# Optimization experiments

Hardware: AMD Instinct MI355X
Metric: run time of the kernel (lower is better)

## Reference

```python
import jax, jax.numpy as jnp
import numpy as np

K = 32
BN_EPS = 1e-5


def _fps(points, n_samples):
    # Sequential farthest point sampling; deterministic start at index 0
    # (torch version uses a random start; math otherwise identical).
    B, N, _ = points.shape

    def step(carry, _):
        dist_min, far = carry                                   # (B,N), (B,)
        c = jnp.take_along_axis(points, far[:, None, None].astype(jnp.int32) * jnp.ones((1, 1, 3), jnp.int32), axis=1)  # (B,1,3)
        d = jnp.sum((points - c) ** 2, axis=2)                  # (B,N)
        dist_min = jnp.minimum(dist_min, d)
        return (dist_min, jnp.argmax(dist_min, axis=1)), far

    init = (jnp.full((B, N), 1e10, points.dtype), jnp.zeros((B,), jnp.int64).astype(jnp.int32))
    _, cent = jax.lax.scan(step, init, None, length=n_samples)  # (n_samples, B)
    return cent.T                                               # (B, n_samples)


def _knn_idx(cntrds, pnts, k):
    # squared euclidean distance (same neighbor ordering as torch.cdist)
    d2 = (jnp.sum(cntrds ** 2, -1)[:, :, None]
          + jnp.sum(pnts ** 2, -1)[:, None, :]
          - 2.0 * jnp.einsum('bsc,bnc->bsn', cntrds, pnts))     # (B,ns,N)
    _, idx = jax.lax.top_k(-d2, k)                              # smallest-k
    return idx                                                  # (B,ns,k)


def _gather(x, idx):
    # x: (B,N,D), idx: (B,...) -> (B,...,D)
    return jax.vmap(lambda a, i: a[i])(x, idx)


def _conv1x1(x, w):
    # x: (B,Cin,ns,k), w: (Cout,Cin)
    return jnp.einsum('oc,bcnk->bonk', w, x)


def _bn_relu(x, g, b):
    # training-mode BatchNorm2d (biased variance over B,ns,k) + ReLU
    mean = jnp.mean(x, axis=(0, 2, 3), keepdims=True)
    var = jnp.var(x, axis=(0, 2, 3), keepdims=True)
    xh = (x - mean) * jax.lax.rsqrt(var + BN_EPS)
    return jax.nn.relu(xh * g[None, :, None, None] + b[None, :, None, None])


def setup_inputs() -> dict:
    key = jax.random.key(0)
    ks = jax.random.split(key, 16)
    B, N = 4, 4096
    s = 0.05
    return {
        'p': jax.random.normal(ks[0], (B, N, 3), jnp.float32),
        'f': jax.random.normal(ks[1], (B, 3, N), jnp.float32),
        'w1': jax.random.normal(ks[2], (256, 6), jnp.float32) * s,
        'w2': jax.random.normal(ks[3], (256, 256), jnp.float32) * s,
        'b2': jax.random.normal(ks[4], (256,), jnp.float32) * s,
        'g2': jnp.ones((256,), jnp.float32),
        'be2': jnp.zeros((256,), jnp.float32),
        'w3': jax.random.normal(ks[5], (512, 512), jnp.float32) * s,
        'g3': jnp.ones((512,), jnp.float32),
        'be3': jnp.zeros((512,), jnp.float32),
        'w4': jax.random.normal(ks[6], (256, 512), jnp.float32) * s,
        'g4': jnp.ones((256,), jnp.float32),
        'be4': jnp.zeros((256,), jnp.float32),
    }


def reference(p, f, w1, w2, b2, g2, be2, w3, g3, be3, w4, g4, be4):
    B, N, _ = p.shape
    ns = N // 4
    idx_c = _fps(p, ns)                                   # (B,ns)
    cntrd = _gather(p, idx_c)                             # (B,ns,3)
    feats = jnp.transpose(f, (0, 2, 1))                   # (B,N,3)
    knn = _knn_idx(cntrd, p, K)                           # (B,ns,K)
    dp = _gather(p, knn)                                  # (B,ns,K,3)
    fj = _gather(feats, knn)                              # (B,ns,K,3)
    x = jnp.transpose(jnp.concatenate([dp, fj], -1), (0, 3, 1, 2))  # (B,6,ns,K)
    # conv1: 6->256 (no bias), 256->256 (bias) + BN + ReLU
    x = _conv1x1(x, w1)
    x = _conv1x1(x, w2) + b2[None, :, None, None]
    x = _bn_relu(x, g2, be2)                              # (B,256,ns,K)
    xm = jnp.max(x, axis=-1, keepdims=True)
    x = jnp.concatenate([jnp.broadcast_to(xm, x.shape), x], axis=1)  # (B,512,ns,K)
    # conv2: 512->512 BN ReLU, 512->256 BN ReLU
    x = _bn_relu(_conv1x1(x, w3), g3, be3)
    x = _bn_relu(_conv1x1(x, w4), g4, be4)
    out_feat = jnp.max(x, axis=-1)                        # (B,256,ns)
    return cntrd, out_feat
```

## Files before the change

### kernel.cpp

```cpp
#include <hip/hip_runtime.h>
#include <hip/hip_bf16.h>

#define B_ 4
#define N_ 4096
#define NS_ 1024
#define KNN_ 32
#define NPOS_ 131072
#define BN_EPS_ 1e-5f

using bf16 = __hip_bfloat16;
typedef unsigned short us;
typedef __attribute__((ext_vector_type(8))) short short8;
typedef __attribute__((ext_vector_type(4))) float f32x4;
typedef unsigned long long ull;

__device__ __forceinline__ float bf2f(bf16 h){ return __bfloat162float(h); }
__device__ __forceinline__ us f2bfbits(float x){
    bf16 h = __float2bfloat16(x);
    return *reinterpret_cast<us*>(&h);
}
__device__ __forceinline__ float bits2f(us u){
    unsigned v = ((unsigned)u)<<16; return __uint_as_float(v);
}
__device__ __forceinline__ void unpack8(uint4 v, float* f){
    f[0]=__uint_as_float((v.x&0xFFFFu)<<16); f[1]=__uint_as_float(v.x&0xFFFF0000u);
    f[2]=__uint_as_float((v.y&0xFFFFu)<<16); f[3]=__uint_as_float(v.y&0xFFFF0000u);
    f[4]=__uint_as_float((v.z&0xFFFFu)<<16); f[5]=__uint_as_float(v.z&0xFFFF0000u);
    f[6]=__uint_as_float((v.w&0xFFFFu)<<16); f[7]=__uint_as_float(v.w&0xFFFF0000u);
}
__device__ __forceinline__ uint4 pack8(const float* f){
    uint4 v;
    v.x = (unsigned)f2bfbits(f[0]) | ((unsigned)f2bfbits(f[1])<<16);
    v.y = (unsigned)f2bfbits(f[2]) | ((unsigned)f2bfbits(f[3])<<16);
    v.z = (unsigned)f2bfbits(f[4]) | ((unsigned)f2bfbits(f[5])<<16);
    v.w = (unsigned)f2bfbits(f[6]) | ((unsigned)f2bfbits(f[7])<<16);
    return v;
}
__device__ __forceinline__ unsigned fmono(float v){
    unsigned u = __float_as_uint(v);
    return (u & 0x80000000u) ? ~u : (u | 0x80000000u);
}

template<int CTRL, int ROWM>
__device__ __forceinline__ float dppmaxf(float x){
    int xi = __float_as_int(x);
    int yi = __builtin_amdgcn_update_dpp(xi, xi, CTRL, ROWM, 0xF, false);
    return fmaxf(x, __int_as_float(yi));
}
template<int CTRL, int ROWM>
__device__ __forceinline__ float dppminf(float x){
    int xi = __float_as_int(x);
    int yi = __builtin_amdgcn_update_dpp(xi, xi, CTRL, ROWM, 0xF, false);
    return fminf(x, __int_as_float(yi));
}
__device__ __forceinline__ float wave_max_f32(float x){
    x = dppmaxf<0x111,0xF>(x);
    x = dppmaxf<0x112,0xF>(x);
    x = dppmaxf<0x114,0xF>(x);
    x = dppmaxf<0x118,0xF>(x);
    x = dppmaxf<0x142,0xA>(x);
    x = dppmaxf<0x143,0xC>(x);
    return __int_as_float(__builtin_amdgcn_readlane(__float_as_int(x), 63));
}
__device__ __forceinline__ float wave_min_f32(float x){
    x = dppminf<0x111,0xF>(x);
    x = dppminf<0x112,0xF>(x);
    x = dppminf<0x114,0xF>(x);
    x = dppminf<0x118,0xF>(x);
    x = dppminf<0x142,0xA>(x);
    x = dppminf<0x143,0xC>(x);
    return __int_as_float(__builtin_amdgcn_readlane(__float_as_int(x), 63));
}
__device__ __forceinline__ float rowsum16(float x){
    x += __int_as_float(__builtin_amdgcn_update_dpp(0, __float_as_int(x), 0x111, 0xF, 0xF, true));
    x += __int_as_float(__builtin_amdgcn_update_dpp(0, __float_as_int(x), 0x112, 0xF, 0xF, true));
    x += __int_as_float(__builtin_amdgcn_update_dpp(0, __float_as_int(x), 0x114, 0xF, 0xF, true));
    x += __int_as_float(__builtin_amdgcn_update_dpp(0, __float_as_int(x), 0x118, 0xF, 0xF, true));
    return x;
}
__device__ __forceinline__ float wave_sum_f32(float x){
    x = rowsum16(x);
    x += __int_as_float(__builtin_amdgcn_update_dpp(0, __float_as_int(x), 0x142, 0xA, 0xF, false));
    x += __int_as_float(__builtin_amdgcn_update_dpp(0, __float_as_int(x), 0x143, 0xC, 0xF, false));
    return __int_as_float(__builtin_amdgcn_readlane(__float_as_int(x), 63));
}
__device__ __forceinline__ float max16(const float* v){
    float a = fmaxf(fmaxf(fmaxf(v[0],v[1]),v[2]),v[3]);
    float b = fmaxf(fmaxf(fmaxf(v[4],v[5]),v[6]),v[7]);
    float c = fmaxf(fmaxf(fmaxf(v[8],v[9]),v[10]),v[11]);
    float d = fmaxf(fmaxf(fmaxf(v[12],v[13]),v[14]),v[15]);
    return fmaxf(fmaxf(a,b), fmaxf(c,d));
}
__device__ __forceinline__ float min16(const float* v){
    float a = fminf(fminf(fminf(v[0],v[1]),v[2]),v[3]);
    float b = fminf(fminf(fminf(v[4],v[5]),v[6]),v[7]);
    float c = fminf(fminf(fminf(v[8],v[9]),v[10]),v[11]);
    float d = fminf(fminf(fminf(v[12],v[13]),v[14]),v[15]);
    return fminf(fminf(a,b), fminf(c,d));
}

#define NSLOT 64

__global__ __launch_bounds__(256) void bn_coef(const float* __restrict__ part,
                                               const float* __restrict__ g,
                                               const float* __restrict__ be,
                                               int chbase, int C,
                                               float2* __restrict__ ab){
    int c = blockIdx.x*256 + threadIdx.x;
    if (c < C){
        const float* ps = part + (size_t)(chbase+c)*2*NSLOT;
        float s = 0.f, q = 0.f;
        #pragma unroll 8
        for (int i=0;i<NSLOT;i++){ s += ps[i]; q += ps[NSLOT+i]; }
        const float inv = 1.0f/(float)NPOS_;
        float mean = s*inv;
        float var  = q*inv - mean*mean;
        float a = g[c]*rsqrtf(var + BN_EPS_);
        ab[c] = make_float2(a, be[c] - mean*a);
    }
}

__global__ __launch_bounds__(256) void mega_kernel(const float* __restrict__ p,
                                                   const float* __restrict__ f,
                                                   float* __restrict__ cntrd,
                                                   float* __restrict__ part,
                                                   int* __restrict__ prog,
                                                   int* __restrict__ w26flag,
                                                   const float* __restrict__ w1,
                                                   const float* __restrict__ w2,
                                                   float* __restrict__ W26,
                                                   const float* __restrict__ b2,
                                                   const float* __restrict__ w3,
                                                   us* __restrict__ whi3,
                                                   const float* __restrict__ w4,
                                                   us* __restrict__ whi4,
                                                   bf16* __restrict__ z2){
    __shared__ float4 pxyz[N_];
    __shared__ ull warr[2][4];
    __shared__ int knnS[32];
    __shared__ float Ws[6][256];
    __shared__ float xs[6][32];
    __shared__ int ciS;
    const int bid = blockIdx.x;
    const int t = threadIdx.x;
    const int lane = t & 63;
    const int wave = t >> 6;

    if (bid < 4){
        const int b = bid;
        const float* pb = p + (size_t)b*N_*3;
        float rx[16], ry[16], rz[16], dist[16];
        #pragma unroll
        for (int j=0;j<16;j++){
            int i = t*16+j;
            float x = pb[i*3+0];
            float y = pb[i*3+1];
            float z = pb[i*3+2];
            rx[j]=x; ry[j]=y; rz[j]=z;
            pxyz[i] = make_float4(x,y,z,0.f);
            dist[j]=1e10f;
        }
        __syncthreads();
        float4 c = pxyz[0];
        if (t==0){
            atomicExch(&prog[b*NS_], 1);
            cntrd[(size_t)(b*NS_)*3+0] = c.x;
            cntrd[(size_t)(b*NS_)*3+1] = c.y;
            cntrd[(size_t)(b*NS_)*3+2] = c.z;
        }
        for (int s=1; s<NS_; s++){
            #pragma unroll
            for (int j=0;j<16;j++){
                float dx = __fsub_rn(rx[j],c.x);
                float dy = __fsub_rn(ry[j],c.y);
                float dz = __fsub_rn(rz[j],c.z);
                float d  = __fadd_rn(__fadd_rn(__fmul_rn(dx,dx),__fmul_rn(dy,dy)),__fmul_rn(dz,dz));
                dist[j] = fminf(dist[j], d);
            }
            float lmax = max16(dist);
            float wmax = wave_max_f32(lmax);
            unsigned msk = 0;
            #pragma unroll
            for (int j=0;j<16;j++) msk |= (dist[j]==wmax) ? (1u<<j) : 0u;
            ull ball = __ballot(msk != 0);
            int srclane = (int)__builtin_ctzll(ball);
            unsigned lmsk = (unsigned)__builtin_amdgcn_readlane((int)msk, srclane);
            int widx = (wave*64 + srclane)*16 + (int)__builtin_ctz(lmsk);
            if (lane==0)
                warr[s&1][wave] = ((ull)__float_as_uint(wmax)<<32) | (0xFFFFFFFFu - (unsigned)widx);
            __syncthreads();
            ull g0 = warr[s&1][0], g1 = warr[s&1][1], g2 = warr[s&1][2], g3 = warr[s&1][3];
            ull ga = g0 > g1 ? g0 : g1;
            ull gb = g2 > g3 ? g2 : g3;
            ull g  = ga > gb ? ga : gb;
            int cur = (int)(0xFFFFFFFFu - (unsigned)(g & 0xFFFFFFFFull));
            c = pxyz[cur];
            if (t==0){
                atomicExch(&prog[b*NS_+s], cur+1);
                cntrd[(size_t)(b*NS_+s)*3+0] = c.x;
                cntrd[(size_t)(b*NS_+s)*3+1] = c.y;
                cntrd[(size_t)(b*NS_+s)*3+2] = c.z;
            }
        }
        return;
    }
    if (bid == 4){
        float acc[6] = {0,0,0,0,0,0};
        for (int k=0;k<256;k++){
            float w2v = w2[t*256+k];
            #pragma unroll
            for (int j=0;j<6;j++) acc[j] = fmaf(w2v, w1[k*6+j], acc[j]);
        }
        #pragma unroll
        for (int j=0;j<6;j++) W26[j*256+t] = acc[j];
        __syncthreads();
        if (t==0){ __threadfence(); atomicExch(w26flag, 1); }
        return;
    }
    if (bid < 1029){
        int i = (bid-5)*256 + t;
        whi3[i] = f2bfbits(w3[i]);
        return;
    }
    if (bid < 1541){
        int i = (bid-1029)*256 + t;
        whi4[i] = f2bfbits(w4[i]);
        return;
    }
    const int wid = bid - 1541;
    const int b = wid & 3;
    const int si = wid >> 2;
    const int sidx = b*NS_ + si;
    const float* pb = p + (size_t)b*N_*3;
    if (t == 0){
        int v;
        while ((v = atomicAdd(&prog[sidx], 0)) == 0) {}
        ciS = v - 1;
    }
    __syncthreads();
    const int ci = ciS;
    float cx = pb[ci*3+0];
    float cy = pb[ci*3+1];
    float cz = pb[ci*3+2];
    float c2 = __fadd_rn(__fadd_rn(__fmul_rn(cx,cx),__fmul_rn(cy,cy)),__fmul_rn(cz,cz));
    float d2[16];
    #pragma unroll
    for (int j=0;j<16;j++){
        int i = t*16+j;
        float x = pb[i*3+0];
        float y = pb[i*3+1];
        float z = pb[i*3+2];
        float p2 = __fadd_rn(__fadd_rn(__fmul_rn(x,x),__fmul_rn(y,y)),__fmul_rn(z,z));
        float dot= __fadd_rn(__fadd_rn(__fmul_rn(cx,x),__fmul_rn(cy,y)),__fmul_rn(cz,z));
        d2[j] = __fsub_rn(__fadd_rn(c2,p2), __fmul_rn(2.0f,dot));
    }
    for (int it=0; it<KNN_; it++){
        float lmin = min16(d2);
        float wmin = wave_min_f32(lmin);
        unsigned msk = 0;
        #pragma unroll
        for (int j=0;j<16;j++) msk |= (d2[j]==wmin) ? (1u<<j) : 0u;
        ull ball = __ballot(msk != 0);
        int srclane = (int)__builtin_ctzll(ball);
        unsigned lmsk = (unsigned)__builtin_amdgcn_readlane((int)msk, srclane);
        int widx = (wave*64 + srclane)*16 + (int)__builtin_ctz(lmsk);
        if (lane==0)
            warr[it&1][wave] = ((ull)fmono(wmin)<<32) | (unsigned)widx;
        __syncthreads();
        ull g0 = warr[it&1][0], g1 = warr[it&1][1], g2 = warr[it&1][2], g3 = warr[it&1][3];
        ull ga = g0 < g1 ? g0 : g1;
        ull gb = g2 < g3 ? g2 : g3;
        ull g  = ga < gb ? ga : gb;
        int idx = (int)(g & 0xFFFFFFFFull);
        if ((idx>>4)==t) d2[idx & 15] = INFINITY;
        if (t==0) knnS[it] = idx;
    }
    if (t == 0){ while (atomicAdd(w26flag, 0) == 0) {} __threadfence(); }
    __syncthreads();
    #pragma unroll
    for (int r=0;r<6;r++) Ws[r][t] = W26[r*256+t];
    if (t < 32){
        int i = knnS[t];
        const float* fb = f + (size_t)b*3*N_;
        xs[0][t] = pb[i*3+0];
        xs[1][t] = pb[i*3+1];
        xs[2][t] = pb[i*3+2];
        xs[3][t] = fb[0*N_+i];
        xs[4][t] = fb[1*N_+i];
        xs[5][t] = fb[2*N_+i];
    }
    __syncthreads();
    float w0=Ws[0][t], w1v=Ws[1][t], w2v=Ws[2][t], w3v=Ws[3][t], w4v=Ws[4][t], w5v=Ws[5][t];
    float bias = b2[t];
    bf16* zrow = z2 + (size_t)t*NPOS_ + (size_t)sidx*KNN_;
    float ssum = 0.f, sq = 0.f;
    for (int k0=0;k0<32;k0+=8){
        float y[8];
        #pragma unroll
        for (int u=0;u<8;u++){
            int k = k0+u;
            float acc = bias;
            acc = fmaf(w0, xs[0][k], acc);
            acc = fmaf(w1v,xs[1][k], acc);
            acc = fmaf(w2v,xs[2][k], acc);
            acc = fmaf(w3v,xs[3][k], acc);
            acc = fmaf(w4v,xs[4][k], acc);
            acc = fmaf(w5v,xs[5][k], acc);
            float vr = bits2f(f2bfbits(acc));
            ssum += vr; sq = fmaf(vr, vr, sq);
            y[u] = acc;
        }
        *reinterpret_cast<uint4*>(zrow + k0) = pack8(y);
    }
    const int slot = wid & (NSLOT-1);
    atomicAdd(&part[(size_t)(t*2+0)*NSLOT + slot], ssum);
    atomicAdd(&part[(size_t)(t*2+1)*NSLOT + slot], sq);
}

__global__ __launch_bounds__(256) void xm_kernel(const bf16* __restrict__ z2raw,
                                                 const float2* __restrict__ ab,
                                                 bf16* __restrict__ xm){
    int gid = blockIdx.x*256 + threadIdx.x;
    int c = gid >> 12;
    int bs = gid & 4095;
    float2 s = ab[c];
    const uint4* xp = reinterpret_cast<const uint4*>(z2raw + (size_t)c*NPOS_ + (size_t)bs*KNN_);
    float m = 0.0f;
    #pragma unroll
    for (int r=0;r<4;r++){
        uint4 v = xp[r];
        float fv[8]; unpack8(v, fv);
        #pragma unroll
        for (int u=0;u<8;u++) m = fmaxf(m, fmaf(fv[u], s.x, s.y));
    }
    xm[(size_t)c*4096 + bs] = __float2bfloat16(m);
}

__global__ __launch_bounds__(256) void gemm128(const float* __restrict__ A, int lda, int aoff,
                                               const bf16* __restrict__ B,
                                               int M, int N, int K,
                                               float* __restrict__ Cf){
    __shared__ float As[16][128];
    __shared__ float Bs[16][128];
    const int tid = threadIdx.x;
    const int tx = tid & 15, ty = tid >> 4;
    const int m0 = blockIdx.y*128, n0 = blockIdx.x*128;
    float acc[8][8];
    #pragma unroll
    for (int i=0;i<8;i++)
        #pragma unroll
        for (int j=0;j<8;j++) acc[i][j]=0.f;
    const int arow = tid >> 1, akg = tid & 1;
    const int bkk = tid >> 4, bng = tid & 15;
    for (int k0=0;k0<K;k0+=16){
        const float* aptr = A + (size_t)(m0+arow)*lda + aoff + k0 + akg*8;
        float4 a0 = *reinterpret_cast<const float4*>(aptr);
        float4 a1 = *reinterpret_cast<const float4*>(aptr+4);
        As[akg*8+0][arow]=a0.x; As[akg*8+1][arow]=a0.y;
        As[akg*8+2][arow]=a0.z; As[akg*8+3][arow]=a0.w;
        As[akg*8+4][arow]=a1.x; As[akg*8+5][arow]=a1.y;
        As[akg*8+6][arow]=a1.z; As[akg*8+7][arow]=a1.w;
        uint4 bv = *reinterpret_cast<const uint4*>(B + (size_t)(k0+bkk)*N + n0 + bng*8);
        float bf[8]; unpack8(bv, bf);
        *reinterpret_cast<float4*>(&Bs[bkk][bng*8+0]) = make_float4(bf[0],bf[1],bf[2],bf[3]);
        *reinterpret_cast<float4*>(&Bs[bkk][bng*8+4]) = make_float4(bf[4],bf[5],bf[6],bf[7]);
        __syncthreads();
        #pragma unroll
        for (int kk=0;kk<16;kk++){
            float a[8], b[8];
            *reinterpret_cast<float4*>(&a[0]) = *reinterpret_cast<float4*>(&As[kk][ty*8+0]);
            *reinterpret_cast<float4*>(&a[4]) = *reinterpret_cast<float4*>(&As[kk][ty*8+4]);
            *reinterpret_cast<float4*>(&b[0]) = *reinterpret_cast<float4*>(&Bs[kk][tx*8+0]);
            *reinterpret_cast<float4*>(&b[4]) = *reinterpret_cast<float4*>(&Bs[kk][tx*8+4]);
            #pragma unroll
            for (int i=0;i<8;i++)
                #pragma unroll
                for (int j=0;j<8;j++)
                    acc[i][j] = fmaf(a[i], b[j], acc[i][j]);
        }
        __syncthreads();
    }
    const int n = n0 + tx*8;
    #pragma unroll
    for (int i=0;i<8;i++){
        int m = m0 + ty*8 + i;
        *reinterpret_cast<float4*>(Cf + (size_t)m*N + n + 0) = make_float4(acc[i][0],acc[i][1],acc[i][2],acc[i][3]);
        *reinterpret_cast<float4*>(Cf + (size_t)m*N + n + 4) = make_float4(acc[i][4],acc[i][5],acc[i][6],acc[i][7]);
    }
}

#define LDK 40
__global__ __launch_bounds__(256) void gemm_mfma(const us* __restrict__ Whi,
                                                 int ldw, int aoff,
                                                 const bf16* __restrict__ act, int K,
                                                 const float2* __restrict__ ab,
                                                 bf16* __restrict__ out,
                                                 const float* __restrict__ t3,
                                                 float* __restrict__ part, int chbase){
    __shared__ __align__(16) us AsH[128*LDK];
    __shared__ __align__(16) us Bs [128*LDK];
    __shared__ float t3s[128][4];
    const us* actu = reinterpret_cast<const us*>(act);
    const int t = threadIdx.x;
    const int m0 = blockIdx.x*128, n0 = blockIdx.y*128;
    const int wave = t>>6, lane = t&63;
    const int wm = wave>>1, wn = wave&1;
    const int q = lane>>4, col = lane&15;

    if (t3 && t < 128){
        const float* src = t3 + (size_t)(m0+t)*4096 + (n0>>5);
        t3s[t][0]=src[0]; t3s[t][1]=src[1]; t3s[t][2]=src[2]; t3s[t][3]=src[3];
    }

    f32x4 acc[4][4];
    #pragma unroll
    for (int i=0;i<4;i++)
        #pragma unroll
        for (int j=0;j<4;j++) acc[i][j] = (f32x4){0.f,0.f,0.f,0.f};

    const int ar = t>>1, ah = t&1;
    const int bn = t&127, bh = t>>7;

    for (int k0=0;k0<K;k0+=32){
        const us* sh = Whi + (size_t)(m0+ar)*ldw + aoff + k0 + ah*16;
        uint4 h0 = *reinterpret_cast<const uint4*>(sh);
        uint4 h1 = *reinterpret_cast<const uint4*>(sh+8);
        *reinterpret_cast<uint4*>(&AsH[ar*LDK + ah*16 + 0]) = h0;
        *reinterpret_cast<uint4*>(&AsH[ar*LDK + ah*16 + 8]) = h1;
        us bvals[16];
        #pragma unroll
        for (int j=0;j<16;j++){
            int k = k0 + bh*16 + j;
            float x = bits2f(actu[(size_t)k*NPOS_ + n0 + bn]);
            float2 s = ab[k];
            bvals[j] = f2bfbits(fmaxf(fmaf(x, s.x, s.y), 0.0f));
        }
        *reinterpret_cast<uint4*>(&Bs[bn*LDK + bh*16 + 0]) = *reinterpret_cast<uint4*>(&bvals[0]);
        *reinterpret_cast<uint4*>(&Bs[bn*LDK + bh*16 + 8]) = *reinterpret_cast<uint4*>(&bvals[8]);
        __syncthreads();
        short8 bf[4], afh[4];
        #pragma unroll
        for (int tn=0;tn<4;tn++)
            bf[tn] = *reinterpret_cast<const short8*>(&Bs[(wn*64+tn*16+col)*LDK + q*8]);
        #pragma unroll
        for (int tm=0;tm<4;tm++)
            afh[tm] = *reinterpret_cast<const short8*>(&AsH[(wm*64+tm*16+col)*LDK + q*8]);
        #pragma unroll
        for (int tm=0;tm<4;tm++)
            #pragma unroll
            for (int tn=0;tn<4;tn++)
                acc[tm][tn] = __builtin_amdgcn_mfma_f32_16x16x32_bf16(afh[tm], bf[tn], acc[tm][tn], 0, 0, 0);
        __syncthreads();
    }
    const int slot = (int)(blockIdx.y & (NSLOT-1));
    #pragma unroll
    for (int tm=0;tm<4;tm++){
        #pragma unroll
        for (int r=0;r<4;r++){
            int m_l = wm*64 + tm*16 + q*4 + r;
            float srow = 0.f, qrow = 0.f;
            #pragma unroll
            for (int tn=0;tn<4;tn++){
                int n_l = wn*64 + tn*16 + col;
                float vv = acc[tm][tn][r];
                if (t3) vv += t3s[m_l][n_l>>5];
                us hb = f2bfbits(vv);
                reinterpret_cast<us*>(out)[(size_t)(m0+m_l)*NPOS_ + n0 + n_l] = hb;
                float vr = bits2f(hb);
                srow += vr; qrow = fmaf(vr, vr, qrow);
            }
            srow = rowsum16(srow);
            qrow = rowsum16(qrow);
            if (col == 15){
                atomicAdd(&part[(size_t)((chbase + m0 + m_l)*2+0)*NSLOT + slot], srow);
                atomicAdd(&part[(size_t)((chbase + m0 + m_l)*2+1)*NSLOT + slot], qrow);
            }
        }
    }
}

__global__ __launch_bounds__(256) void final_kernel(const bf16* __restrict__ z4,
                                                    const float* __restrict__ part,
                                                    const float* __restrict__ g4,
                                                    const float* __restrict__ be4,
                                                    float* __restrict__ out){
    __shared__ float abS[2];
    const int t = threadIdx.x;
    const int c = (blockIdx.x >> 2) & 255;
    const int b = blockIdx.x >> 10;
    const int s = ((blockIdx.x & 3) << 8) | t;
    if (t < 64){
        float ss = part[(size_t)((768+c)*2+0)*NSLOT + t];
        float qq = part[(size_t)((768+c)*2+1)*NSLOT + t];
        ss = wave_sum_f32(ss);
        qq = wave_sum_f32(qq);
        if (t==0){
            const float inv = 1.0f/(float)NPOS_;
            float mean = ss*inv;
            float var  = qq*inv - mean*mean;
            float a = g4[c]*rsqrtf(var + BN_EPS_);
            abS[0] = a; abS[1] = be4[c] - mean*a;
        }
    }
    __syncthreads();
    const float a = abS[0], bb = abS[1];
    const int bsi = b*NS_ + s;
    const uint4* zp = reinterpret_cast<const uint4*>(z4 + (size_t)c*NPOS_ + (size_t)bsi*KNN_);
    float m = 0.0f;
    #pragma unroll
    for (int r=0;r<4;r++){
        uint4 v = zp[r];
        float fv[8]; unpack8(v, fv);
        #pragma unroll
        for (int u=0;u<8;u++) m = fmaxf(m, fmaf(fv[u], a, bb));
    }
    out[(size_t)(b*256 + c)*NS_ + s] = m;
}

extern "C" void kernel_launch(void* const* d_in, const int* in_sizes, int n_in,
                              void* d_out, int out_size, void* d_ws, size_t ws_size,
                              hipStream_t stream) {
    const float* p   = (const float*)d_in[0];
    const float* f   = (const float*)d_in[1];
    const float* w1  = (const float*)d_in[2];
    const float* w2  = (const float*)d_in[3];
    const float* b2  = (const float*)d_in[4];
    const float* g2  = (const float*)d_in[5];
    const float* be2 = (const float*)d_in[6];
    const float* w3  = (const float*)d_in[7];
    const float* g3  = (const float*)d_in[8];
    const float* be3 = (const float*)d_in[9];
    const float* w4  = (const float*)d_in[10];
    const float* g4  = (const float*)d_in[11];
    const float* be4 = (const float*)d_in[12];

    char* ws = (char*)d_ws;
    float*  W26  = (float*)(ws + 540672);
    float2* ab2  = (float2*)(ws + 555008);
    float2* ab3  = (float2*)(ws + 557056);
    us* whi3 = (us*)(ws + 561152);
    us* whi4 = (us*)(ws + 1609728);
    float*  t3   = (float*)(ws + 2134016);
    bf16*   z2   = (bf16*)(ws + 10522624);
    bf16*   xm   = (bf16*)(ws + 77631488);
    bf16*   z3   = (bf16*)(ws + 79728640);
    float*  part = (float*)(ws + 213946368);
    int*    prog = (int*)(ws + 214470656);
    int*    w26flag = (int*)(ws + 214487040);
    bf16*   z4   = z2;

    float* out_cntrd = (float*)d_out;
    float* out_feat  = (float*)d_out + (size_t)B_*NS_*3;

    hipMemsetAsync(ws + 213946368, 0, 540676, stream);
    mega_kernel<<<5637, 256, 0, stream>>>(p, f, out_cntrd, part, prog, w26flag,
                                          w1, w2, W26, b2,
                                          w3, whi3, w4, whi4, z2);
    bn_coef<<<1, 256, 0, stream>>>(part, g2, be2, 0, 256, ab2);
    xm_kernel<<<4096, 256, 0, stream>>>(z2, ab2, xm);
    gemm128<<<dim3(32,4), 256, 0, stream>>>(w3, 512, 0, xm, 512, 4096, 256, t3);
    gemm_mfma<<<dim3(4,1024), 256, 0, stream>>>(whi3, 512, 256, z2, 256, ab2, z3, t3, part, 256);
    bn_coef<<<2, 256, 0, stream>>>(part, g3, be3, 256, 512, ab3);
    gemm_mfma<<<dim3(2,1024), 256, 0, stream>>>(whi4, 512, 0, z3, 512, ab3, z4, nullptr, part, 768);
    final_kernel<<<4096, 256, 0, stream>>>(z4, part, g4, be4, out_feat);
}
```

Baseline: 1.056 ms.

## Track per-neighbourhood raw max/min to skip re-reading full activations for max-pool

Since BN followed by ReLU is a monotone affine map per channel, the max over K neighbours can be taken from the raw max (positive scale) or raw min (negative scale). The producers now emit per-position max and min in bf16, and xm_kernel and final_kernel read those instead of the full 32-wide rows. The last GEMM no longer writes its full z4 output. Separately, the FPS blocks get raised wave priority and the spin-wait loops get s_sleep. The trade is extra reductions and stores inside the producer epilogues in exchange for much less read traffic.

```diff
diff --git a/kernel.cpp b/kernel.cpp
--- a/kernel.cpp
+++ b/kernel.cpp
@@ -76,6 +76,20 @@
     x += __int_as_float(__builtin_amdgcn_update_dpp(0, __float_as_int(x), 0x112, 0xF, 0xF, true));
     x += __int_as_float(__builtin_amdgcn_update_dpp(0, __float_as_int(x), 0x114, 0xF, 0xF, true));
     x += __int_as_float(__builtin_amdgcn_update_dpp(0, __float_as_int(x), 0x118, 0xF, 0xF, true));
+    return x;
+}
+__device__ __forceinline__ float rowmax16(float x){
+    x = dppmaxf<0x111,0xF>(x);
+    x = dppmaxf<0x112,0xF>(x);
+    x = dppmaxf<0x114,0xF>(x);
+    x = dppmaxf<0x118,0xF>(x);
+    return x;
+}
+__device__ __forceinline__ float rowmin16(float x){
+    x = dppminf<0x111,0xF>(x);
+    x = dppminf<0x112,0xF>(x);
+    x = dppminf<0x114,0xF>(x);
+    x = dppminf<0x118,0xF>(x);
     return x;
 }
 __device__ __forceinline__ float wave_sum_f32(float x){
@@ -134,7 +148,9 @@
                                                    us* __restrict__ whi3,
                                                    const float* __restrict__ w4,
                                                    us* __restrict__ whi4,
-                                                   bf16* __restrict__ z2){
+                                                   bf16* __restrict__ z2,
+                                                   us* __restrict__ mx2,
+                                                   us* __restrict__ mn2){
     __shared__ float4 pxyz[N_];
     __shared__ ull warr[2][4];
     __shared__ int knnS[32];
@@ -147,6 +163,7 @@
     const int wave = t >> 6;
 
     if (bid < 4){
+        __builtin_amdgcn_s_setprio(3);
         const int b = bid;
         const float* pb = p + (size_t)b*N_*3;
         float rx[16], ry[16], rz[16], dist[16];
@@ -234,7 +251,7 @@
     const float* pb = p + (size_t)b*N_*3;
     if (t == 0){
         int v;
-        while ((v = atomicAdd(&prog[sidx], 0)) == 0) {}
+        while ((v = atomicAdd(&prog[sidx], 0)) == 0) { __builtin_amdgcn_s_sleep(8); }
         ciS = v - 1;
     }
     __syncthreads();
@@ -275,7 +292,7 @@
         if ((idx>>4)==t) d2[idx & 15] = INFINITY;
         if (t==0) knnS[it] = idx;
     }
-    if (t == 0){ while (atomicAdd(w26flag, 0) == 0) {} __threadfence(); }
+    if (t == 0){ while (atomicAdd(w26flag, 0) == 0) { __builtin_amdgcn_s_sleep(8); } __threadfence(); }
     __syncthreads();
     #pragma unroll
     for (int r=0;r<6;r++) Ws[r][t] = W26[r*256+t];
@@ -294,6 +311,7 @@
     float bias = b2[t];
     bf16* zrow = z2 + (size_t)t*NPOS_ + (size_t)sidx*KNN_;
     float ssum = 0.f, sq = 0.f;
+    float mxv = -3.4e38f, mnv = 3.4e38f;
     for (int k0=0;k0<32;k0+=8){
         float y[8];
         #pragma unroll
@@ -308,32 +326,28 @@
             acc = fmaf(w5v,xs[5][k], acc);
             float vr = bits2f(f2bfbits(acc));
             ssum += vr; sq = fmaf(vr, vr, sq);
+            mxv = fmaxf(mxv, vr); mnv = fminf(mnv, vr);
             y[u] = acc;
         }
         *reinterpret_cast<uint4*>(zrow + k0) = pack8(y);
     }
+    mx2[(size_t)t*4096 + sidx] = f2bfbits(mxv);
+    mn2[(size_t)t*4096 + sidx] = f2bfbits(mnv);
     const int slot = wid & (NSLOT-1);
     atomicAdd(&part[(size_t)(t*2+0)*NSLOT + slot], ssum);
     atomicAdd(&part[(size_t)(t*2+1)*NSLOT + slot], sq);
 }
 
-__global__ __launch_bounds__(256) void xm_kernel(const bf16* __restrict__ z2raw,
+__global__ __launch_bounds__(256) void xm_kernel(const us* __restrict__ mx2,
+                                                 const us* __restrict__ mn2,
                                                  const float2* __restrict__ ab,
                                                  bf16* __restrict__ xm){
     int gid = blockIdx.x*256 + threadIdx.x;
     int c = gid >> 12;
-    int bs = gid & 4095;
     float2 s = ab[c];
-    const uint4* xp = reinterpret_cast<const uint4*>(z2raw + (size_t)c*NPOS_ + (size_t)bs*KNN_);
-    float m = 0.0f;
-    #pragma unroll
-    for (int r=0;r<4;r++){
-        uint4 v = xp[r];
-        float fv[8]; unpack8(v, fv);
-        #pragma unroll
-        for (int u=0;u<8;u++) m = fmaxf(m, fmaf(fv[u], s.x, s.y));
-    }
-    xm[(size_t)c*4096 + bs] = __float2bfloat16(m);
+    float x = (s.x >= 0.f) ? bits2f(mx2[gid]) : bits2f(mn2[gid]);
+    float m = fmaxf(fmaf(x, s.x, s.y), 0.0f);
+    xm[gid] = __float2bfloat16(m);
 }
 
 __global__ __launch_bounds__(256) void gemm128(const float* __restrict__ A, int lda, int aoff,
@@ -396,7 +410,9 @@
                                                  const float2* __restrict__ ab,
                                                  bf16* __restrict__ out,
                                                  const float* __restrict__ t3,
-                                                 float* __restrict__ part, int chbase){
+                                                 float* __restrict__ part, int chbase,
+                                                 us* __restrict__ mxout,
+                                                 us* __restrict__ mnout){
     __shared__ __align__(16) us AsH[128*LDK];
     __shared__ __align__(16) us Bs [128*LDK];
     __shared__ float t3s[128][4];
@@ -459,14 +475,17 @@
         for (int r=0;r<4;r++){
             int m_l = wm*64 + tm*16 + q*4 + r;
             float srow = 0.f, qrow = 0.f;
+            float vr4[4];
             #pragma unroll
             for (int tn=0;tn<4;tn++){
                 int n_l = wn*64 + tn*16 + col;
                 float vv = acc[tm][tn][r];
                 if (t3) vv += t3s[m_l][n_l>>5];
                 us hb = f2bfbits(vv);
-                reinterpret_cast<us*>(out)[(size_t)(m0+m_l)*NPOS_ + n0 + n_l] = hb;
+                if (!mxout)
+                    reinterpret_cast<us*>(out)[(size_t)(m0+m_l)*NPOS_ + n0 + n_l] = hb;
                 float vr = bits2f(hb);
+                vr4[tn] = vr;
                 srow += vr; qrow = fmaf(vr, vr, qrow);
             }
             srow = rowsum16(srow);
@@ -475,11 +494,26 @@
                 atomicAdd(&part[(size_t)((chbase + m0 + m_l)*2+0)*NSLOT + slot], srow);
                 atomicAdd(&part[(size_t)((chbase + m0 + m_l)*2+1)*NSLOT + slot], qrow);
             }
-        }
-    }
-}
-
-__global__ __launch_bounds__(256) void final_kernel(const bf16* __restrict__ z4,
+            if (mxout){
+                #pragma unroll
+                for (int h=0;h<2;h++){
+                    float mxl = fmaxf(vr4[2*h], vr4[2*h+1]);
+                    float mnl = fminf(vr4[2*h], vr4[2*h+1]);
+                    mxl = rowmax16(mxl);
+                    mnl = rowmin16(mnl);
+                    if (col == 15){
+                        int bsi = (n0>>5) + wn*2 + h;
+                        mxout[(size_t)(m0+m_l)*4096 + bsi] = f2bfbits(mxl);
+                        mnout[(size_t)(m0+m_l)*4096 + bsi] = f2bfbits(mnl);
+                    }
+                }
+            }
+        }
+    }
+}
+
+__global__ __launch_bounds__(256) void final_kernel(const us* __restrict__ mx4,
+                                                    const us* __restrict__ mn4,
                                                     const float* __restrict__ part,
                                                     const float* __restrict__ g4,
                                                     const float* __restrict__ be4,
@@ -505,16 +539,8 @@
     __syncthreads();
     const float a = abS[0], bb = abS[1];
     const int bsi = b*NS_ + s;
-    const uint4* zp = reinterpret_cast<const uint4*>(z4 + (size_t)c*NPOS_ + (size_t)bsi*KNN_);
-    float m = 0.0f;
-    #pragma unroll
-    for (int r=0;r<4;r++){
-        uint4 v = zp[r];
-        float fv[8]; unpack8(v, fv);
-        #pragma unroll
-        for (int u=0;u<8;u++) m = fmaxf(m, fmaf(fv[u], a, bb));
-    }
-    out[(size_t)(b*256 + c)*NS_ + s] = m;
+    float x = (a >= 0.f) ? bits2f(mx4[(size_t)c*4096 + bsi]) : bits2f(mn4[(size_t)c*4096 + bsi]);
+    out[(size_t)(b*256 + c)*NS_ + s] = fmaxf(fmaf(x, a, bb), 0.0f);
 }
 
 extern "C" void kernel_launch(void* const* d_in, const int* in_sizes, int n_in,
@@ -541,13 +567,16 @@
     us* whi3 = (us*)(ws + 561152);
     us* whi4 = (us*)(ws + 1609728);
     float*  t3   = (float*)(ws + 2134016);
+    us*     mx2  = (us*)(ws + 2134016);
+    us*     mn2  = (us*)(ws + 2134016 + 2097152);
     bf16*   z2   = (bf16*)(ws + 10522624);
+    us*     mx4  = (us*)(ws + 10522624);
+    us*     mn4  = (us*)(ws + 10522624 + 2097152);
     bf16*   xm   = (bf16*)(ws + 77631488);
     bf16*   z3   = (bf16*)(ws + 79728640);
     float*  part = (float*)(ws + 213946368);
     int*    prog = (int*)(ws + 214470656);
     int*    w26flag = (int*)(ws + 214487040);
-    bf16*   z4   = z2;
 
     float* out_cntrd = (float*)d_out;
     float* out_feat  = (float*)d_out + (size_t)B_*NS_*3;
@@ -555,12 +584,14 @@
     hipMemsetAsync(ws + 213946368, 0, 540676, stream);
     mega_kernel<<<5637, 256, 0, stream>>>(p, f, out_cntrd, part, prog, w26flag,
                                           w1, w2, W26, b2,
-                                          w3, whi3, w4, whi4, z2);
+                                          w3, whi3, w4, whi4, z2, mx2, mn2);
     bn_coef<<<1, 256, 0, stream>>>(part, g2, be2, 0, 256, ab2);
-    xm_kernel<<<4096, 256, 0, stream>>>(z2, ab2, xm);
+    xm_kernel<<<4096, 256, 0, stream>>>(mx2, mn2, ab2, xm);
     gemm128<<<dim3(32,4), 256, 0, stream>>>(w3, 512, 0, xm, 512, 4096, 256, t3);
-    gemm_mfma<<<dim3(4,1024), 256, 0, stream>>>(whi3, 512, 256, z2, 256, ab2, z3, t3, part, 256);
+    gemm_mfma<<<dim3(4,1024), 256, 0, stream>>>(whi3, 512, 256, z2, 256, ab2, z3, t3, part, 256,
+                                                nullptr, nullptr);
     bn_coef<<<2, 256, 0, stream>>>(part, g3, be3, 256, 512, ab3);
-    gemm_mfma<<<dim3(2,1024), 256, 0, stream>>>(whi4, 512, 0, z3, 512, ab3, z4, nullptr, part, 768);
-    final_kernel<<<4096, 256, 0, stream>>>(z4, part, g4, be4, out_feat);
-}
+    gemm_mfma<<<dim3(2,1024), 256, 0, stream>>>(whi4, 512, 0, z3, 512, ab3, nullptr, nullptr, part, 768,
+                                                mx4, mn4);
+    final_kernel<<<4096, 256, 0, stream>>>(mx4, mn4, part, g4, be4, out_feat);
+}
```

After: 1.049 ms. No clear change (-0.7%).
